# Kernel optimization log

Hardware: AMD Instinct MI355X
Metric: run time of the kernel (lower is better)

The kernel has to match this reference:

```python
import jax, jax.numpy as jnp
import numpy as np

T, B, C = 2048, 4, 1024
H, K = 16, 15
PAD_L = 14  # causal: padding_l = K - 1


def setup_inputs() -> dict:
    key = jax.random.key(0)
    k1, k2 = jax.random.split(key)
    x = jax.random.normal(k1, (T, B, C), dtype=jnp.float32)
    # xavier_uniform for Linear(C, H*K): bound = sqrt(6/(fan_in+fan_out))
    bound = float(np.sqrt(6.0 / (C + H * K)))
    Wlin = jax.random.uniform(k2, (H * K, C), dtype=jnp.float32, minval=-bound, maxval=bound)
    return {"x": x, "Wlin": Wlin}


def reference(x, Wlin):
    # x: (T, B, C); Wlin: (H*K, C) -- weight_linear with no bias
    t, b, c = x.shape
    r = c // H  # channels per head
    # Generate per-position filters: (T, B, H, K)
    w = jnp.einsum('tbc,kc->tbk', x, Wlin).reshape(t, b, H, K)
    # weight_softmax=True: normalize over kernel taps
    w = jax.nn.softmax(w, axis=-1)
    # unfold1d: pad left PAD_L, right K-1-PAD_L along time, take K shifted views
    xp = jnp.pad(x, ((PAD_L, K - 1 - PAD_L), (0, 0), (0, 0)))
    # (T, B, C, K): tap k at output t reads padded position t+k
    xu = jnp.stack([xp[k:k + t] for k in range(K)], axis=-1)
    xu = xu.reshape(t, b, H, r, K)
    # batched tiny matmul: (R x K) @ (K x 1) per (t, b, h)
    out = jnp.einsum('tbhrk,tbhk->tbhr', xu, w)
    return out.reshape(t, b, c)
```

## Files before the change

### kernel.cpp

```cpp
#include <hip/hip_runtime.h>
#include <hip/hip_bf16.h>


#define T_DIM 2048
#define B_DIM 4
#define C_DIM 1024
#define H_DIM 16
#define K_TAPS 15
#define R_DIM 64
#define N_DIM (H_DIM * K_TAPS)
#define M_DIM (T_DIM * B_DIM)
#define SM_STRIDE 244

typedef __attribute__((ext_vector_type(8))) short bf16x8;
typedef __attribute__((ext_vector_type(4))) float f32x4;

__device__ __forceinline__ unsigned short f2bf(float f) {
    union { float f; unsigned u; } v; v.f = f;
    return (unsigned short)((v.u + 0x7FFFu + ((v.u >> 16) & 1u)) >> 16);
}

__global__ __launch_bounds__(256) void convert_w(
    const float* __restrict__ W, unsigned short* __restrict__ Wbf)
{
    int i = (blockIdx.x * 256 + threadIdx.x) * 4;
    float4 v = *reinterpret_cast<const float4*>(W + i);
    ushort4 o;
    o.x = f2bf(v.x); o.y = f2bf(v.y); o.z = f2bf(v.z); o.w = f2bf(v.w);
    *reinterpret_cast<ushort4*>(Wbf + i) = o;
}

__global__ __launch_bounds__(256) void gemm_softmax_mfma(
    const float* __restrict__ x, const unsigned short* __restrict__ Wbf,
    float* __restrict__ wbuf)
{
    __shared__ float sm[4][16][SM_STRIDE];

    const int tid = threadIdx.x;
    const int w   = tid >> 6;
    const int l   = tid & 63;
    const int m0  = blockIdx.x * 16;
    const int row = l & 15;
    const int kg  = l >> 4;

    f32x4 acc[15];
    #pragma unroll
    for (int nt = 0; nt < 15; ++nt) acc[nt] = (f32x4){0.f, 0.f, 0.f, 0.f};

    const float* xp = x + (size_t)(m0 + row) * C_DIM + w * 256 + kg * 8;
    const unsigned short* wp = Wbf + (size_t)row * C_DIM + w * 256 + kg * 8;

    #pragma unroll 2
    for (int ks = 0; ks < 8; ++ks) {
        const int k = ks * 32;
        float4 a0 = *reinterpret_cast<const float4*>(xp + k);
        float4 a1 = *reinterpret_cast<const float4*>(xp + k + 4);
        bf16x8 af;
        af[0] = (short)f2bf(a0.x); af[1] = (short)f2bf(a0.y);
        af[2] = (short)f2bf(a0.z); af[3] = (short)f2bf(a0.w);
        af[4] = (short)f2bf(a1.x); af[5] = (short)f2bf(a1.y);
        af[6] = (short)f2bf(a1.z); af[7] = (short)f2bf(a1.w);
        bf16x8 bfr[15];
        #pragma unroll
        for (int nt = 0; nt < 15; ++nt)
            bfr[nt] = *reinterpret_cast<const bf16x8*>(wp + (size_t)nt * 16 * C_DIM + k);
        #pragma unroll
        for (int nt = 0; nt < 15; ++nt)
            acc[nt] = __builtin_amdgcn_mfma_f32_16x16x32_bf16(af, bfr[nt], acc[nt], 0, 0, 0);
    }

    #pragma unroll
    for (int nt = 0; nt < 15; ++nt)
        #pragma unroll
        for (int j = 0; j < 4; ++j)
            sm[w][kg * 4 + j][nt * 16 + row] = acc[nt][j];
    __syncthreads();

    const int r = tid >> 4;
    const int h = tid & 15;
    float s[K_TAPS];
    #pragma unroll
    for (int kk = 0; kk < K_TAPS; ++kk) {
        const int c = h * K_TAPS + kk;
        s[kk] = sm[0][r][c] + sm[1][r][c] + sm[2][r][c] + sm[3][r][c];
    }
    float mx = s[0];
    #pragma unroll
    for (int kk = 1; kk < K_TAPS; ++kk) mx = fmaxf(mx, s[kk]);
    float sum = 0.f;
    #pragma unroll
    for (int kk = 0; kk < K_TAPS; ++kk) {
        s[kk] = __expf(s[kk] - mx);
        sum += s[kk];
    }
    const float inv = 1.f / sum;
    float* dst = wbuf + (size_t)(m0 + r) * N_DIM + h * K_TAPS;
    #pragma unroll
    for (int kk = 0; kk < K_TAPS; ++kk) dst[kk] = s[kk] * inv;
}

__global__ __launch_bounds__(256) void conv_kernel(
    const float* __restrict__ x, const float* __restrict__ wbuf,
    float* __restrict__ out)
{
    __shared__ float xs[64 + K_TAPS - 1][R_DIM];

    const int tid = threadIdx.x;
    const int t0 = blockIdx.x * 64;
    const int bh = blockIdx.y;
    const int b = bh >> 4;
    const int h = bh & 15;
    const int cbase = h * R_DIM;

    for (int idx = tid; idx < (64 + K_TAPS - 1) * 16; idx += 256) {
        int rrow = idx >> 4, q = idx & 15;
        int t = t0 - (K_TAPS - 1) + rrow;
        float4 v = (t >= 0)
            ? *reinterpret_cast<const float4*>(x + ((size_t)t * B_DIM + b) * C_DIM + cbase + q * 4)
            : (float4){0.f, 0.f, 0.f, 0.f};
        *reinterpret_cast<float4*>(&xs[rrow][q * 4]) = v;
    }
    __syncthreads();

    const int r = tid & 63;
    const int tg = __builtin_amdgcn_readfirstlane(tid >> 6);

    float xv[31];
    #pragma unroll
    for (int j = 0; j < 31; ++j) xv[j] = xs[tg * 16 + j][r];

    float accv[16];
    #pragma unroll
    for (int i = 0; i < 16; ++i) accv[i] = 0.f;

    #pragma unroll
    for (int i = 0; i < 16; ++i) {
        const int t = t0 + tg * 16 + i;
        const float* wv = wbuf + ((size_t)t * B_DIM + b) * N_DIM + h * K_TAPS;
        #pragma unroll
        for (int k = 0; k < K_TAPS; ++k)
            accv[i] += wv[k] * xv[i + k];
    }

    #pragma unroll
    for (int i = 0; i < 16; ++i) {
        const int t = t0 + tg * 16 + i;
        out[((size_t)t * B_DIM + b) * C_DIM + cbase + r] = accv[i];
    }
}

extern "C" void kernel_launch(void* const* d_in, const int* in_sizes, int n_in,
                              void* d_out, int out_size, void* d_ws, size_t ws_size,
                              hipStream_t stream) {
    const float* x    = (const float*)d_in[0];
    const float* Wlin = (const float*)d_in[1];
    float* out  = (float*)d_out;

    float* wbuf = (float*)d_ws;
    unsigned short* Wbf = (unsigned short*)((char*)d_ws + (size_t)M_DIM * N_DIM * sizeof(float));

    convert_w<<<(N_DIM * C_DIM) / (256 * 4), 256, 0, stream>>>(Wlin, Wbf);
    gemm_softmax_mfma<<<M_DIM / 16, 256, 0, stream>>>(x, Wbf, wbuf);
    conv_kernel<<<dim3(T_DIM / 64, B_DIM * H_DIM), 256, 0, stream>>>(x, wbuf, out);
}
```

Measured before the change: 127.9 us.

## Double-buffer GEMM operand loads and pad softmax weights to 16 for vector stores

The GEMM main loop now prefetches the next k-step's B fragments and x values into registers while MFMAs run on the current ones. The kernel also gets a launch_bounds occupancy hint of 2 blocks. The softmax output is padded from 15 to 16 floats per head so it can be written with aligned float4 stores, and the conv kernel reads the padded layout. The prefetch doubles register use for the B fragments, which may conflict with the occupancy hint and cause spills, and the padding adds a small amount of extra workspace traffic.

```diff
diff --git a/kernel.cpp b/kernel.cpp
--- a/kernel.cpp
+++ b/kernel.cpp
@@ -8,8 +8,8 @@
 #define H_DIM 16
 #define K_TAPS 15
 #define R_DIM 64
-#define N_DIM (H_DIM * K_TAPS)
-#define M_DIM (T_DIM * B_DIM)
+#define N_DIM 240
+#define M_DIM 8192
 #define SM_STRIDE 244
 
 typedef __attribute__((ext_vector_type(8))) short bf16x8;
@@ -30,73 +30,90 @@
     *reinterpret_cast<ushort4*>(Wbf + i) = o;
 }
 
-__global__ __launch_bounds__(256) void gemm_softmax_mfma(
+__global__ __launch_bounds__(256, 2) void gemm_softmax_mfma(
     const float* __restrict__ x, const unsigned short* __restrict__ Wbf,
-    float* __restrict__ wbuf)
+    float* __restrict__ wout)
 {
     __shared__ float sm[4][16][SM_STRIDE];
 
     const int tid = threadIdx.x;
-    const int w   = tid >> 6;
+    const int wv  = tid >> 6;
     const int l   = tid & 63;
     const int m0  = blockIdx.x * 16;
     const int row = l & 15;
     const int kg  = l >> 4;
 
+    const float* xp = x + (size_t)(m0 + row) * C_DIM + wv * 256 + kg * 8;
+    const unsigned short* wp = Wbf + (size_t)row * C_DIM + wv * 256 + kg * 8;
+
     f32x4 acc[15];
     #pragma unroll
     for (int nt = 0; nt < 15; ++nt) acc[nt] = (f32x4){0.f, 0.f, 0.f, 0.f};
 
-    const float* xp = x + (size_t)(m0 + row) * C_DIM + w * 256 + kg * 8;
-    const unsigned short* wp = Wbf + (size_t)row * C_DIM + w * 256 + kg * 8;
+    bf16x8 bcur[15];
+    #pragma unroll
+    for (int nt = 0; nt < 15; ++nt)
+        bcur[nt] = *reinterpret_cast<const bf16x8*>(wp + (size_t)nt * 16 * C_DIM);
+    float4 ac0 = *reinterpret_cast<const float4*>(xp);
+    float4 ac1 = *reinterpret_cast<const float4*>(xp + 4);
 
-    #pragma unroll 2
-    for (int ks = 0; ks < 8; ++ks) {
-        const int k = ks * 32;
-        float4 a0 = *reinterpret_cast<const float4*>(xp + k);
-        float4 a1 = *reinterpret_cast<const float4*>(xp + k + 4);
+    #pragma unroll
+    for (int sub = 0; sub < 8; ++sub) {
+        bf16x8 bnxt[15];
+        float4 an0, an1;
+        if (sub < 7) {
+            const int kn = (sub + 1) * 32;
+            #pragma unroll
+            for (int nt = 0; nt < 15; ++nt)
+                bnxt[nt] = *reinterpret_cast<const bf16x8*>(wp + (size_t)nt * 16 * C_DIM + kn);
+            an0 = *reinterpret_cast<const float4*>(xp + kn);
+            an1 = *reinterpret_cast<const float4*>(xp + kn + 4);
+        }
         bf16x8 af;
-        af[0] = (short)f2bf(a0.x); af[1] = (short)f2bf(a0.y);
-        af[2] = (short)f2bf(a0.z); af[3] = (short)f2bf(a0.w);
-        af[4] = (short)f2bf(a1.x); af[5] = (short)f2bf(a1.y);
-        af[6] = (short)f2bf(a1.z); af[7] = (short)f2bf(a1.w);
-        bf16x8 bfr[15];
+        af[0] = (short)f2bf(ac0.x); af[1] = (short)f2bf(ac0.y);
+        af[2] = (short)f2bf(ac0.z); af[3] = (short)f2bf(ac0.w);
+        af[4] = (short)f2bf(ac1.x); af[5] = (short)f2bf(ac1.y);
+        af[6] = (short)f2bf(ac1.z); af[7] = (short)f2bf(ac1.w);
         #pragma unroll
         for (int nt = 0; nt < 15; ++nt)
-            bfr[nt] = *reinterpret_cast<const bf16x8*>(wp + (size_t)nt * 16 * C_DIM + k);
-        #pragma unroll
-        for (int nt = 0; nt < 15; ++nt)
-            acc[nt] = __builtin_amdgcn_mfma_f32_16x16x32_bf16(af, bfr[nt], acc[nt], 0, 0, 0);
+            acc[nt] = __builtin_amdgcn_mfma_f32_16x16x32_bf16(af, bcur[nt], acc[nt], 0, 0, 0);
+        if (sub < 7) {
+            #pragma unroll
+            for (int nt = 0; nt < 15; ++nt) bcur[nt] = bnxt[nt];
+            ac0 = an0; ac1 = an1;
+        }
     }
 
     #pragma unroll
     for (int nt = 0; nt < 15; ++nt)
         #pragma unroll
         for (int j = 0; j < 4; ++j)
-            sm[w][kg * 4 + j][nt * 16 + row] = acc[nt][j];
+            sm[wv][kg * 4 + j][nt * 16 + row] = acc[nt][j];
     __syncthreads();
 
-    const int r = tid >> 4;
-    const int h = tid & 15;
+    const int rr = tid >> 4;
+    const int hh = tid & 15;
     float s[K_TAPS];
     #pragma unroll
     for (int kk = 0; kk < K_TAPS; ++kk) {
-        const int c = h * K_TAPS + kk;
-        s[kk] = sm[0][r][c] + sm[1][r][c] + sm[2][r][c] + sm[3][r][c];
+        const int c = hh * K_TAPS + kk;
+        s[kk] = sm[0][rr][c] + sm[1][rr][c] + sm[2][rr][c] + sm[3][rr][c];
     }
     float mx = s[0];
     #pragma unroll
     for (int kk = 1; kk < K_TAPS; ++kk) mx = fmaxf(mx, s[kk]);
     float sum = 0.f;
     #pragma unroll
-    for (int kk = 0; kk < K_TAPS; ++kk) {
-        s[kk] = __expf(s[kk] - mx);
-        sum += s[kk];
-    }
+    for (int kk = 0; kk < K_TAPS; ++kk) { s[kk] = __expf(s[kk] - mx); sum += s[kk]; }
     const float inv = 1.f / sum;
-    float* dst = wbuf + (size_t)(m0 + r) * N_DIM + h * K_TAPS;
+    float o[16];
     #pragma unroll
-    for (int kk = 0; kk < K_TAPS; ++kk) dst[kk] = s[kk] * inv;
+    for (int kk = 0; kk < K_TAPS; ++kk) o[kk] = s[kk] * inv;
+    o[15] = 0.f;
+    float* dst = wout + ((size_t)(m0 + rr)) * (H_DIM * 16) + hh * 16;
+    #pragma unroll
+    for (int q = 0; q < 4; ++q)
+        *reinterpret_cast<float4*>(dst + q * 4) = *reinterpret_cast<const float4*>(&o[q * 4]);
 }
 
 __global__ __launch_bounds__(256) void conv_kernel(
@@ -136,10 +153,10 @@
     #pragma unroll
     for (int i = 0; i < 16; ++i) {
         const int t = t0 + tg * 16 + i;
-        const float* wv = wbuf + ((size_t)t * B_DIM + b) * N_DIM + h * K_TAPS;
+        const float* wrow = wbuf + ((size_t)t * B_DIM + b) * (H_DIM * 16) + h * 16;
         #pragma unroll
         for (int k = 0; k < K_TAPS; ++k)
-            accv[i] += wv[k] * xv[i + k];
+            accv[i] += wrow[k] * xv[i + k];
     }
 
     #pragma unroll
@@ -154,12 +171,12 @@
                               hipStream_t stream) {
     const float* x    = (const float*)d_in[0];
     const float* Wlin = (const float*)d_in[1];
-    float* out  = (float*)d_out;
+    float* out = (float*)d_out;
 
-    float* wbuf = (float*)d_ws;
-    unsigned short* Wbf = (unsigned short*)((char*)d_ws + (size_t)M_DIM * N_DIM * sizeof(float));
+    float* wout = (float*)d_ws;
+    unsigned short* Wbf = (unsigned short*)((char*)d_ws + (size_t)M_DIM * H_DIM * 16 * sizeof(float));
 
     convert_w<<<(N_DIM * C_DIM) / (256 * 4), 256, 0, stream>>>(Wlin, Wbf);
-    gemm_softmax_mfma<<<M_DIM / 16, 256, 0, stream>>>(x, Wbf, wbuf);
-    conv_kernel<<<dim3(T_DIM / 64, B_DIM * H_DIM), 256, 0, stream>>>(x, wbuf, out);
+    gemm_softmax_mfma<<<M_DIM / 16, 256, 0, stream>>>(x, Wbf, wout);
+    conv_kernel<<<dim3(T_DIM / 64, B_DIM * H_DIM), 256, 0, stream>>>(x, wout, out);
 }
```

New measurement: 128.7 us. Within noise of the previous version (+0.6%).
